# Performance work log

Hardware: AMD Instinct MI355X
Metric: run time of the kernel (lower is better)

## Reference

```python
import jax, jax.numpy as jnp
import numpy as np

B, N, D_PATCH = 32, 196, 768
TKN, QK, H, HID = 768, 64, 12, 3072
K_STEPS = 12
ALPHA = 1.0
BETA = 1.0 / (QK ** 0.5)
EPS = 1e-5


def setup_inputs() -> dict:
    key = jax.random.key(0)
    ks = jax.random.split(key, 8)
    w_std = 0.002
    return {
        "x": jax.random.normal(ks[0], (B, N, D_PATCH), jnp.float32),
        "w_enc": jax.random.normal(ks[1], (TKN, D_PATCH), jnp.float32) * 0.02,
        "b_enc": jnp.zeros((TKN,), jnp.float32),
        "cls_tok": jnp.ones((1, 1, TKN), jnp.float32),
        "pos": jax.random.normal(ks[2], (1, N + 1, TKN), jnp.float32) * w_std,
        "eln_gamma": jnp.ones((1,), jnp.float32),
        "eln_bias": jnp.zeros((TKN,), jnp.float32),
        "wq": jax.random.normal(ks[3], (H, QK, TKN), jnp.float32) * w_std,
        "wk": jax.random.normal(ks[4], (H, QK, TKN), jnp.float32) * w_std,
        "w_hop": jax.random.normal(ks[5], (HID, TKN), jnp.float32) * 0.02,
        "dec_ln_w": jnp.ones((TKN,), jnp.float32),
        "dec_ln_b": jnp.zeros((TKN,), jnp.float32),
        "w_dec": jax.random.normal(ks[6], (D_PATCH, TKN), jnp.float32) * 0.02,
        "b_dec": jnp.zeros((D_PATCH,), jnp.float32),
    }


def _energy(g, wq, wk, w_hop):
    # attention energy: non-softmax, -1/beta * sum logsumexp(beta * A)
    q = jnp.einsum('bnd,hzd->bnhz', g, wq)
    k = jnp.einsum('bnd,hzd->bnhz', g, wk)
    A = jnp.einsum('bqhz,bkhz->bhqk', q, k)  # [B,H,N+1,N+1]
    e_attn = (-1.0 / BETA) * jnp.sum(jax.nn.logsumexp(BETA * A, axis=-1))
    # Hopfield energy: -0.5 * sum relu(g W^T)^2
    h = jnp.einsum('bnd,fd->bnf', g, w_hop)  # [B,N+1,HID]
    e_hop = -0.5 * jnp.sum(jax.nn.relu(h) ** 2)
    return e_attn + e_hop


def _energy_ln(x, gamma, bias):
    xm = x - x.mean(-1, keepdims=True)
    o = xm / jnp.sqrt((xm ** 2).mean(-1, keepdims=True) + EPS)
    return gamma * o + bias


def _layernorm(x, w, b):
    mu = x.mean(-1, keepdims=True)
    xm = x - mu
    var = (xm ** 2).mean(-1, keepdims=True)
    return xm / jnp.sqrt(var + EPS) * w + b


def reference(x, w_enc, b_enc, cls_tok, pos, eln_gamma, eln_bias,
              wq, wk, w_hop, dec_ln_w, dec_ln_b, w_dec, b_dec):
    # encode: Linear(d_patch -> tkn)
    t = jnp.einsum('bnd,td->bnt', x, w_enc) + b_enc
    # prepend cls, add positional encoding
    cls = jnp.broadcast_to(cls_tok, (t.shape[0], 1, TKN))
    t = jnp.concatenate([cls, t], axis=1) + pos  # [B, N+1, TKN]

    grad_e = jax.grad(lambda g: _energy(g, wq, wk, w_hop))
    for _ in range(K_STEPS):  # fixed unroll over time steps (single block)
        g = _energy_ln(t, eln_gamma, eln_bias)
        t = t - ALPHA * grad_e(g)

    # decode: LayerNorm + Linear(tkn -> d_patch)
    y = _layernorm(t, dec_ln_w, dec_ln_b)
    y = jnp.einsum('bnt,dt->bnd', y, w_dec) + b_dec
    return y[:, 1:]  # drop cls token (use_cls=False)
```

## Files before the change

### kernel.cpp

```cpp
#include <hip/hip_runtime.h>
#include <hip/hip_bf16.h>

typedef __hip_bfloat16 bf16;
typedef short s8 __attribute__((ext_vector_type(8)));
typedef short sv4 __attribute__((ext_vector_type(4)));
typedef float f4 __attribute__((ext_vector_type(4)));

#define BETA 0.125f
#define EPS 1e-5f

__device__ __forceinline__ void gld16(const void* g, void* l){
    __builtin_amdgcn_global_load_lds(
        (const __attribute__((address_space(1))) void*)g,
        (__attribute__((address_space(3))) void*)l, 16, 0, 0);
}

__global__ __launch_bounds__(256) void f2b_k(const float* __restrict__ in, bf16* __restrict__ out, long n){
    long i = (long)blockIdx.x*256 + threadIdx.x;
    if (i < n) out[i] = __float2bfloat16(in[i]);
}
__global__ __launch_bounds__(256) void padx_k(const float* __restrict__ x, bf16* __restrict__ xb){
    long i = (long)blockIdx.x*256 + threadIdx.x;
    if (i >= 6400L*768) return;
    long row = i / 768;
    xb[i] = (row < 6272) ? __float2bfloat16(x[i]) : __float2bfloat16(0.f);
}
__global__ __launch_bounds__(256) void tr_k(const short* __restrict__ Bi, short* __restrict__ Bo){
    __shared__ short t[32][33];
    int i0 = blockIdx.x*32, j0 = blockIdx.y*32;
    int li = threadIdx.x & 31, lj = threadIdx.x >> 5;
    #pragma unroll
    for (int r=0;r<4;r++) t[lj+8*r][li] = Bi[(long)(i0+lj+8*r)*768 + j0+li];
    __syncthreads();
    #pragma unroll
    for (int r=0;r<4;r++) Bo[(long)(j0+lj+8*r)*4608 + i0+li] = t[li][lj+8*r];
}

__global__ __launch_bounds__(256) void cls_k(const float* __restrict__ cls, const float* __restrict__ pos,
                                             float* __restrict__ t){
    int i = blockIdx.x*256 + threadIdx.x;
    int b = i / 768, c = i % 768;
    t[((long)b*197)*768 + c] = cls[c] + pos[c];
}

template<int MODE>
__global__ __launch_bounds__(256) void big_gemm(
    const short* __restrict__ A, int lda,
    const short* __restrict__ B, int ldb,
    float* __restrict__ Cf, bf16* __restrict__ Cb, int ldc,
    int K, int Nn, int Nm, int relu0, long zoff,
    const float* __restrict__ bias, const float* __restrict__ pos)
{
    const int f = blockIdx.x;
    const int npg = 16*Nn;
    const int grp = f / npg;
    const int first_m = grp*16;
    const int gs = (Nm - first_m < 16) ? (Nm - first_m) : 16;
    const int rem = f % npg;
    const int bm = first_m + rem % gs;
    const int bn = rem / gs;

    __shared__ short lsA[8192];
    __shared__ short lsB[8192];
    const int tid = threadIdx.x;
    const int w = tid>>6, l = tid&63;
    const int m0 = bm*128, n0 = bn*128;
    const int srow = tid>>2;
    const int qglob = ((tid&3) - (tid>>3)) & 3;
    const int scol = qglob*8;
    int koff, Ks;
    if (MODE==1){ Ks = K>>1; koff = blockIdx.z * Ks; Cf += (size_t)blockIdx.z * zoff; }
    else        { Ks = K;    koff = 0; }
    const short* pa = A + (size_t)(m0+srow)*lda + koff + scol;
    const short* pb = B + (size_t)(n0+srow)*ldb + koff + scol;
    short* laP = lsA + w*512;
    short* lbP = lsB + w*512;
    const int wm = (w>>1)*64, wn = (w&1)*64;
    const int fr = l&15, fq = ((l>>4) + (fr>>1) & 3)*8;
    f4 acc[4][4] = {};
    const int nk = Ks>>6;
    for (int kt=0; kt<nk; kt++){
        const size_t ko = (size_t)kt*64;
        const size_t ra = 64*(size_t)lda, rb = 64*(size_t)ldb;
        gld16(pa + ko,           laP);
        gld16(pa + ko + ra,      laP + 2048);
        gld16(pa + ko + 32,      laP + 4096);
        gld16(pa + ko + 32 + ra, laP + 6144);
        gld16(pb + ko,           lbP);
        gld16(pb + ko + rb,      lbP + 2048);
        gld16(pb + ko + 32,      lbP + 4096);
        gld16(pb + ko + 32 + rb, lbP + 6144);
        __syncthreads();
        #pragma unroll
        for (int ks=0; ks<2; ks++){
            s8 af[4], bfr[4];
            #pragma unroll
            for (int i=0;i<4;i++) af[i]  = *(const s8*)(lsA + ks*4096 + (wm+i*16+fr)*32 + fq);
            #pragma unroll
            for (int j=0;j<4;j++) bfr[j] = *(const s8*)(lsB + ks*4096 + (wn+j*16+fr)*32 + fq);
            #pragma unroll
            for (int i=0;i<4;i++)
                #pragma unroll
                for (int j=0;j<4;j++)
                    acc[i][j] = __builtin_amdgcn_mfma_f32_16x16x32_bf16(af[i], bfr[j], acc[i][j], 0,0,0);
        }
        __syncthreads();
    }
    const int er = (l>>4)*4;
    const int ec = l&15;
    #pragma unroll
    for (int i=0;i<4;i++){
        #pragma unroll
        for (int j=0;j<4;j++){
            int gr0 = m0 + wm + i*16 + er;
            int gc  = n0 + wn + j*16 + ec;
            #pragma unroll
            for (int r=0;r<4;r++){
                float v = acc[i][j][r];
                int gr = gr0 + r;
                if (MODE==0){
                    if (gc >= relu0) v = v>0.f ? v : 0.f;
                    Cb[(size_t)gr*ldc + gc] = __float2bfloat16(v);
                } else if (MODE==1){
                    Cf[(size_t)gr*ldc + gc] = v;
                } else if (MODE==2){
                    if (gr < 6272){
                        int b = gr/196, n = gr%196;
                        Cf[((size_t)b*197 + n + 1)*768 + gc] = v + bias[gc] + pos[(long)(n+1)*768+gc];
                    }
                } else {
                    if (gr < 6272) Cf[(size_t)gr*ldc + gc] = v + bias[gc];
                }
            }
        }
    }
}

__global__ __launch_bounds__(256) void pack_k(const short* __restrict__ qkh,
                                              short* __restrict__ qT, short* __restrict__ kT){
    __shared__ short tq[64][65];
    __shared__ short tk[64][65];
    const int bh = blockIdx.x, b = bh/12, h = bh%12;
    const int mc = blockIdx.y*64;
    const int tid = threadIdx.x;
    #pragma unroll
    for (int e=0;e<16;e++){
        int i = tid + e*256; int r = i>>6, c = i&63;
        int mg = mc + r;
        short vq = 0, vk = 0;
        if (mg < 197){
            size_t base = (size_t)(b*197+mg)*4608 + h*64 + c;
            vq = qkh[base]; vk = qkh[base+768];
        }
        tq[r][c] = vq; tk[r][c] = vk;
    }
    __syncthreads();
    #pragma unroll
    for (int e=0;e<16;e++){
        int i = tid + e*256; int zr = i>>6, cm = i&63;
        size_t o = (size_t)bh*16384 + (size_t)zr*256 + mc + cm;
        qT[o] = tq[cm][zr];
        kT[o] = tk[cm][zr];
    }
}

__global__ __launch_bounds__(256) void attn_k(
    short* __restrict__ qkh, const short* __restrict__ qT, const short* __restrict__ kT)
{
    __shared__ short Pl[64*232];
    __shared__ short Ptl[208*72];
    const int bh = blockIdx.x, b = bh/12, h = bh%12;
    const int tid = threadIdx.x, w = tid>>6, l = tid&63;
    const int lr = l&15, lq = l>>4;
    const size_t qcol = (size_t)h*64, kcol = 768 + qcol;
    const size_t rbase = (size_t)b*197*4608;
    const short* qTp = qT + (size_t)bh*16384;
    const short* kTp = kT + (size_t)bh*16384;

    for (int i=tid; i<64*16; i+=256){ int r=i>>4, c=208+(i&15); Pl[r*232+c]=0; }

    f4 ak[13];
    #pragma unroll
    for (int t=0;t<13;t++) ak[t] = (f4){0.f,0.f,0.f,0.f};

    for (int iter=0; iter<4; iter++){
        const int m0 = iter*64;
        f4 S[13];
        #pragma unroll
        for (int t=0;t<13;t++) S[t] = (f4){0.f,0.f,0.f,0.f};
        const int mrow = m0 + w*16 + lr;
        #pragma unroll
        for (int ks=0; ks<2; ks++){
            s8 af = *(const s8*)(qkh + rbase + (size_t)mrow*4608 + qcol + ks*32 + lq*8);
            #pragma unroll
            for (int t=0;t<13;t++){
                s8 bf = *(const s8*)(qkh + rbase + (size_t)(t*16+lr)*4608 + kcol + ks*32 + lq*8);
                S[t] = __builtin_amdgcn_mfma_f32_16x16x32_bf16(af, bf, S[t], 0,0,0);
            }
        }
        __syncthreads();
        const int mbase = w*16 + lq*4;
        #pragma unroll
        for (int r=0;r<4;r++){
            float mx = -1e30f;
            #pragma unroll
            for (int t=0;t<13;t++){
                float v = S[t][r]*BETA;
                if (t==12 && lr>=5) v = -1e30f;
                S[t][r] = v;
                mx = fmaxf(mx, v);
            }
            mx = fmaxf(mx, __shfl_xor(mx,1,64)); mx = fmaxf(mx, __shfl_xor(mx,2,64));
            mx = fmaxf(mx, __shfl_xor(mx,4,64)); mx = fmaxf(mx, __shfl_xor(mx,8,64));
            float sm = 0.f;
            #pragma unroll
            for (int t=0;t<13;t++){ float e = __expf(S[t][r]-mx); S[t][r]=e; sm+=e; }
            sm += __shfl_xor(sm,1,64); sm += __shfl_xor(sm,2,64);
            sm += __shfl_xor(sm,4,64); sm += __shfl_xor(sm,8,64);
            float inv = 1.f/sm;
            bool valid = (m0 + mbase + r) < 197;
            #pragma unroll
            for (int t=0;t<13;t++) S[t][r] = valid ? S[t][r]*inv : 0.f;
        }
        #pragma unroll
        for (int t=0;t<13;t++){
            int c = t*16 + lr;
            short pb[4];
            #pragma unroll
            for (int r=0;r<4;r++){
                bf16 bv = __float2bfloat16(S[t][r]);
                pb[r] = *(short*)&bv;
                Pl[(mbase+r)*232 + c] = pb[r];
            }
            *(sv4*)(Ptl + c*72 + mbase) = (sv4){pb[0],pb[1],pb[2],pb[3]};
        }
        __syncthreads();
        f4 aq[4];
        #pragma unroll
        for (int t=0;t<4;t++) aq[t] = (f4){0.f,0.f,0.f,0.f};
        #pragma unroll
        for (int ks=0; ks<7; ks++){
            s8 af = *(const s8*)(kTp + (w*16+lr)*256 + ks*32 + lq*8);
            #pragma unroll
            for (int mt=0;mt<4;mt++){
                s8 bf = *(const s8*)(Pl + (mt*16+lr)*232 + ks*32 + lq*8);
                aq[mt] = __builtin_amdgcn_mfma_f32_16x16x32_bf16(af, bf, aq[mt], 0,0,0);
            }
        }
        #pragma unroll
        for (int mt=0;mt<4;mt++){
            int mg = m0 + mt*16 + lr;
            if (mg < 197){
                sv4 pv;
                #pragma unroll
                for (int r=0;r<4;r++){ bf16 bv=__float2bfloat16(aq[mt][r]); pv[r]=*(short*)&bv; }
                *(sv4*)(qkh + rbase + (size_t)mg*4608 + qcol + w*16 + lq*4) = pv;
            }
        }
        #pragma unroll
        for (int ks=0; ks<2; ks++){
            s8 bf = *(const s8*)(qTp + (w*16+lr)*256 + m0 + ks*32 + lq*8);
            #pragma unroll
            for (int t=0;t<13;t++){
                s8 af = *(const s8*)(Ptl + (t*16+lr)*72 + ks*32 + lq*8);
                ak[t] = __builtin_amdgcn_mfma_f32_16x16x32_bf16(af, bf, ak[t], 0,0,0);
            }
        }
    }
    #pragma unroll
    for (int t=0;t<13;t++){
        #pragma unroll
        for (int r=0;r<4;r++){
            int n = t*16 + lq*4 + r;
            if (n < 197)
                *(bf16*)(qkh + rbase + (size_t)n*4608 + kcol + w*16 + lr) = __float2bfloat16(ak[t][r]);
        }
    }
}

__global__ __launch_bounds__(256) void ln_k(
    float* __restrict__ in, bf16* __restrict__ out,
    const float* __restrict__ p0, const float* __restrict__ p1,
    const float* __restrict__ scale, const float* __restrict__ bias,
    int scalar_scale, int rowmap, int addp, int writet)
{
    int r = blockIdx.x;
    long src = rowmap ? ((long)(r/196)*197 + r%196 + 1) : (long)r;
    float* xr = in + src*768;
    int tid = threadIdx.x;
    float v0 = xr[tid], v1 = xr[tid+256], v2 = xr[tid+512];
    if (addp){
        const float* a = p0 + src*768;
        const float* b = p1 + src*768;
        v0 += a[tid]     + b[tid];
        v1 += a[tid+256] + b[tid+256];
        v2 += a[tid+512] + b[tid+512];
        if (writet){ xr[tid]=v0; xr[tid+256]=v1; xr[tid+512]=v2; }
    }
    __shared__ float red[4];
    float s = v0+v1+v2;
    #pragma unroll
    for (int o=1;o<64;o<<=1) s += __shfl_xor(s, o, 64);
    if ((tid&63)==0) red[tid>>6] = s;
    __syncthreads();
    float mu = (red[0]+red[1]+red[2]+red[3]) * (1.f/768.f);
    float d0=v0-mu, d1=v1-mu, d2=v2-mu;
    float q = d0*d0 + d1*d1 + d2*d2;
    #pragma unroll
    for (int o=1;o<64;o<<=1) q += __shfl_xor(q, o, 64);
    __syncthreads();
    if ((tid&63)==0) red[tid>>6] = q;
    __syncthreads();
    float ms = (red[0]+red[1]+red[2]+red[3]) * (1.f/768.f);
    float inv = rsqrtf(ms + EPS);
    bf16* o_ = out + (long)r*768;
    float s0 = scalar_scale ? scale[0] : scale[tid];
    float s1 = scalar_scale ? s0 : scale[tid+256];
    float s2 = scalar_scale ? s0 : scale[tid+512];
    o_[tid]     = __float2bfloat16(d0*inv*s0 + bias[tid]);
    o_[tid+256] = __float2bfloat16(d1*inv*s1 + bias[tid+256]);
    o_[tid+512] = __float2bfloat16(d2*inv*s2 + bias[tid+512]);
}

extern "C" void kernel_launch(void* const* d_in, const int* in_sizes, int n_in,
                              void* d_out, int out_size, void* d_ws, size_t ws_size,
                              hipStream_t stream) {
    const float* x       = (const float*)d_in[0];
    const float* w_enc   = (const float*)d_in[1];
    const float* b_enc   = (const float*)d_in[2];
    const float* cls_tok = (const float*)d_in[3];
    const float* pos     = (const float*)d_in[4];
    const float* eln_g   = (const float*)d_in[5];
    const float* eln_b   = (const float*)d_in[6];
    const float* wq      = (const float*)d_in[7];
    const float* wk      = (const float*)d_in[8];
    const float* w_hop   = (const float*)d_in[9];
    const float* dln_w   = (const float*)d_in[10];
    const float* dln_b   = (const float*)d_in[11];
    const float* w_dec   = (const float*)d_in[12];
    const float* b_dec   = (const float*)d_in[13];
    float* out = (float*)d_out;

    float* t_  = (float*)d_ws;
    bf16* g_   = (bf16*)(t_ + 6400L*768);
    bf16* qkh  = g_ + 6400L*768;
    bf16* qT   = qkh + 6400L*4608;
    bf16* kT   = qT + 384L*16384;
    float* p0  = (float*)(kT + 384L*16384);
    float* p1  = p0 + 6400L*768;
    bf16* B1   = (bf16*)(p1 + 6400L*768);
    bf16* B2   = B1 + 4608L*768;
    bf16* we_  = B2 + 768L*4608;
    bf16* wd_  = we_ + 768L*768;

    dim3 blk(256);
    const long ZOFF = 6400L*768;

    f2b_k<<<dim3((589824+255)/256),  blk, 0, stream>>>(wq,    B1,          589824);
    f2b_k<<<dim3((589824+255)/256),  blk, 0, stream>>>(wk,    B1+589824,   589824);
    f2b_k<<<dim3((2359296+255)/256), blk, 0, stream>>>(w_hop, B1+1179648, 2359296);
    f2b_k<<<dim3((589824+255)/256),  blk, 0, stream>>>(w_enc, we_,         589824);
    f2b_k<<<dim3((589824+255)/256),  blk, 0, stream>>>(w_dec, wd_,         589824);
    tr_k<<<dim3(144,24), blk, 0, stream>>>((const short*)B1, (short*)B2);
    padx_k<<<dim3((int)((6400L*768+255)/256)), blk, 0, stream>>>(x, g_);

    cls_k<<<dim3(96), blk, 0, stream>>>(cls_tok, pos, t_);
    big_gemm<2><<<dim3(300), blk, 0, stream>>>((const short*)g_, 768, (const short*)we_, 768,
                                               t_, nullptr, 768, 768, 6, 50, 0, 0, b_enc, pos);

    for (int step=0; step<12; step++){
        ln_k<<<dim3(6304), blk, 0, stream>>>(t_, g_, p0, p1, eln_g, eln_b, 1, 0, step>0, 1);
        big_gemm<0><<<dim3(1800), blk, 0, stream>>>((const short*)g_, 768, (const short*)B1, 768,
                                                    nullptr, qkh, 4608, 768, 36, 50, 1536, 0, nullptr, nullptr);
        pack_k<<<dim3(384,4), blk, 0, stream>>>((const short*)qkh, (short*)qT, (short*)kT);
        attn_k<<<dim3(384), blk, 0, stream>>>((short*)qkh, (const short*)qT, (const short*)kT);
        big_gemm<1><<<dim3(300,1,2), blk, 0, stream>>>((const short*)qkh, 4608, (const short*)B2, 4608,
                                                       p0, nullptr, 768, 4608, 6, 50, 0, ZOFF, nullptr, nullptr);
    }

    ln_k<<<dim3(6272), blk, 0, stream>>>(t_, g_, p0, p1, dln_w, dln_b, 0, 1, 1, 0);
    big_gemm<3><<<dim3(300), blk, 0, stream>>>((const short*)g_, 768, (const short*)wd_, 768,
                                               out, nullptr, 768, 768, 6, 50, 0, 0, b_dec, nullptr);
}
```

Baseline: 2.640 ms.

## Add 256x128 triple-buffered ring GEMM with 3-way split-K for step loop

Adds a new 512-thread GEMM kernel with a 256x128 block tile, a three-slot LDS ring buffer fed by direct global-to-LDS loads, and swizzled layouts. It replaces the QKV/hidden projection GEMM and the backward GEMM inside the 12-step loop. The backward GEMM moves from 2-way to 3-way split-K, writing a third partial into the qT buffer, and the layernorm now sums three partials. The larger tile and deeper prefetch aim to raise MFMA utilisation and hide load latency. The costs are lower occupancy, heavier LDS use, and one extra partial-sum read per step.

```diff
diff --git a/kernel.cpp b/kernel.cpp
--- a/kernel.cpp
+++ b/kernel.cpp
@@ -136,6 +136,130 @@
     }
 }
 
+template<int MODE>
+__global__ __launch_bounds__(512, 2) void ring_gemm(
+    const short* __restrict__ A, int lda,
+    const short* __restrict__ B, int ldb,
+    float* __restrict__ Cf, float* __restrict__ Cf2,
+    bf16* __restrict__ Cb, int ldc,
+    int K, int Nn, int Nm, int relu0, long zoff)
+{
+    const int f = blockIdx.x;
+    const int npg = 16*Nn;
+    const int grp = f / npg;
+    const int first_m = grp*16;
+    const int gs = (Nm - first_m < 16) ? (Nm - first_m) : 16;
+    const int rem = f % npg;
+    const int bm = first_m + rem % gs;
+    const int bn = rem / gs;
+
+    __shared__ short lsA[49152];
+    __shared__ short lsB[24576];
+    const int tid = threadIdx.x;
+    const int w = tid>>6, l = tid&63;
+    const int m0 = bm*256, n0 = bn*128;
+
+    int Ks, koff;
+    float* Cp = Cf;
+    if (MODE==1){
+        Ks = K/3; koff = blockIdx.z * Ks;
+        Cp = (blockIdx.z==2) ? Cf2 : Cf + (size_t)blockIdx.z * zoff;
+    } else { Ks = K; koff = 0; }
+    const int NT = Ks>>6;
+
+    const short* sA[4]; const short* sB[2];
+    #pragma unroll
+    for (int j=0;j<4;j++){
+        int c = j*512 + tid;
+        int p = c>>10, r = (c>>2)&255, qd = c&3;
+        int qs = (qd - (r>>1)) & 3;
+        sA[j] = A + (size_t)(m0+r)*lda + koff + p*32 + qs*8;
+    }
+    #pragma unroll
+    for (int j=0;j<2;j++){
+        int c = j*512 + tid;
+        int p = c>>9, r = (c>>2)&127, qd = c&3;
+        int qs = (qd - (r>>1)) & 3;
+        sB[j] = B + (size_t)(n0+r)*ldb + koff + p*32 + qs*8;
+    }
+
+    const int wm = (w>>1)*64, wn = (w&1)*64;
+    const int fr = l&15;
+    const int fq = (((l>>4) + (fr>>1)) & 3)*8;
+    f4 acc[4][4] = {};
+
+    #define STAGE(T, SL) do{ \
+        const size_t ko_ = (size_t)(T)*64; \
+        short* dA_ = lsA + (SL)*16384 + w*512; \
+        short* dB_ = lsB + (SL)*8192  + w*512; \
+        gld16(sA[0]+ko_, dA_);       gld16(sA[1]+ko_, dA_+4096); \
+        gld16(sA[2]+ko_, dA_+8192);  gld16(sA[3]+ko_, dA_+12288); \
+        gld16(sB[0]+ko_, dB_);       gld16(sB[1]+ko_, dB_+4096); \
+    }while(0)
+
+    STAGE(0, 0);
+    if (NT > 1) STAGE(1, 1);
+    if (NT > 1) asm volatile("s_waitcnt vmcnt(6)" ::: "memory");
+    else        asm volatile("s_waitcnt vmcnt(0)" ::: "memory");
+    __builtin_amdgcn_s_barrier();
+    __builtin_amdgcn_sched_barrier(0);
+
+    int s = 0;
+    for (int t=0; t<NT; t++){
+        if (t+2 < NT){
+            int s2 = s+2; if (s2>=3) s2 -= 3;
+            STAGE(t+2, s2);
+        }
+        const short* aP = lsA + s*16384;
+        const short* bP = lsB + s*8192;
+        #pragma unroll
+        for (int ks=0; ks<2; ks++){
+            s8 af[4], bfr[4];
+            #pragma unroll
+            for (int i=0;i<4;i++) af[i]  = *(const s8*)(aP + ks*8192 + (wm+i*16+fr)*32 + fq);
+            #pragma unroll
+            for (int j=0;j<4;j++) bfr[j] = *(const s8*)(bP + ks*4096 + (wn+j*16+fr)*32 + fq);
+            __builtin_amdgcn_s_setprio(1);
+            #pragma unroll
+            for (int i=0;i<4;i++)
+                #pragma unroll
+                for (int j=0;j<4;j++)
+                    acc[i][j] = __builtin_amdgcn_mfma_f32_16x16x32_bf16(af[i], bfr[j], acc[i][j], 0,0,0);
+            __builtin_amdgcn_s_setprio(0);
+        }
+        if (t == NT-1) break;
+        __builtin_amdgcn_sched_barrier(0);
+        if (t+2 < NT) asm volatile("s_waitcnt vmcnt(6)" ::: "memory");
+        else          asm volatile("s_waitcnt vmcnt(0)" ::: "memory");
+        __builtin_amdgcn_s_barrier();
+        __builtin_amdgcn_sched_barrier(0);
+        s = (s==2) ? 0 : s+1;
+    }
+    #undef STAGE
+
+    const int er = (l>>4)*4;
+    const int ec = l&15;
+    #pragma unroll
+    for (int i=0;i<4;i++){
+        #pragma unroll
+        for (int j=0;j<4;j++){
+            int gr0 = m0 + wm + i*16 + er;
+            int gc  = n0 + wn + j*16 + ec;
+            #pragma unroll
+            for (int r=0;r<4;r++){
+                float v = acc[i][j][r];
+                int gr = gr0 + r;
+                if (MODE==0){
+                    if (gc >= relu0) v = v>0.f ? v : 0.f;
+                    Cb[(size_t)gr*ldc + gc] = __float2bfloat16(v);
+                } else {
+                    Cp[(size_t)gr*ldc + gc] = v;
+                }
+            }
+        }
+    }
+}
+
 __global__ __launch_bounds__(256) void pack_k(const short* __restrict__ qkh,
                                               short* __restrict__ qT, short* __restrict__ kT){
     __shared__ short tq[64][65];
@@ -280,7 +404,7 @@
 
 __global__ __launch_bounds__(256) void ln_k(
     float* __restrict__ in, bf16* __restrict__ out,
-    const float* __restrict__ p0, const float* __restrict__ p1,
+    const float* __restrict__ p0, const float* __restrict__ p1, const float* __restrict__ p2,
     const float* __restrict__ scale, const float* __restrict__ bias,
     int scalar_scale, int rowmap, int addp, int writet)
 {
@@ -292,9 +416,10 @@
     if (addp){
         const float* a = p0 + src*768;
         const float* b = p1 + src*768;
-        v0 += a[tid]     + b[tid];
-        v1 += a[tid+256] + b[tid+256];
-        v2 += a[tid+512] + b[tid+512];
+        const float* c = p2 + src*768;
+        v0 += a[tid]     + b[tid]     + c[tid];
+        v1 += a[tid+256] + b[tid+256] + c[tid+256];
+        v2 += a[tid+512] + b[tid+512] + c[tid+512];
         if (writet){ xr[tid]=v0; xr[tid+256]=v1; xr[tid+512]=v2; }
     }
     __shared__ float red[4];
@@ -352,6 +477,7 @@
     bf16* B2   = B1 + 4608L*768;
     bf16* we_  = B2 + 768L*4608;
     bf16* wd_  = we_ + 768L*768;
+    float* p2  = (float*)qT;
 
     dim3 blk(256);
     const long ZOFF = 6400L*768;
@@ -369,16 +495,16 @@
                                                t_, nullptr, 768, 768, 6, 50, 0, 0, b_enc, pos);
 
     for (int step=0; step<12; step++){
-        ln_k<<<dim3(6304), blk, 0, stream>>>(t_, g_, p0, p1, eln_g, eln_b, 1, 0, step>0, 1);
-        big_gemm<0><<<dim3(1800), blk, 0, stream>>>((const short*)g_, 768, (const short*)B1, 768,
-                                                    nullptr, qkh, 4608, 768, 36, 50, 1536, 0, nullptr, nullptr);
+        ln_k<<<dim3(6304), blk, 0, stream>>>(t_, g_, p0, p1, p2, eln_g, eln_b, 1, 0, step>0, 1);
+        ring_gemm<0><<<dim3(900), dim3(512), 0, stream>>>((const short*)g_, 768, (const short*)B1, 768,
+                                                          nullptr, nullptr, qkh, 4608, 768, 36, 25, 1536, 0);
         pack_k<<<dim3(384,4), blk, 0, stream>>>((const short*)qkh, (short*)qT, (short*)kT);
         attn_k<<<dim3(384), blk, 0, stream>>>((short*)qkh, (const short*)qT, (const short*)kT);
-        big_gemm<1><<<dim3(300,1,2), blk, 0, stream>>>((const short*)qkh, 4608, (const short*)B2, 4608,
-                                                       p0, nullptr, 768, 4608, 6, 50, 0, ZOFF, nullptr, nullptr);
-    }
-
-    ln_k<<<dim3(6272), blk, 0, stream>>>(t_, g_, p0, p1, dln_w, dln_b, 0, 1, 1, 0);
+        ring_gemm<1><<<dim3(150,1,3), dim3(512), 0, stream>>>((const short*)qkh, 4608, (const short*)B2, 4608,
+                                                              p0, p2, nullptr, 768, 4608, 6, 25, 0, ZOFF);
+    }
+
+    ln_k<<<dim3(6272), blk, 0, stream>>>(t_, g_, p0, p1, p2, dln_w, dln_b, 0, 1, 1, 0);
     big_gemm<3><<<dim3(300), blk, 0, stream>>>((const short*)g_, 768, (const short*)wd_, 768,
                                                out, nullptr, 768, 768, 6, 50, 0, 0, b_dec, nullptr);
 }
```

Result: slower. 3.118 ms (+18.1%).
